# Optimization experiments

Measured on AMD Instinct MI355X. Metric: run time of the kernel, lower is better.

## Reference

```python
import jax, jax.numpy as jnp
import numpy as np

FIELD_NUM = 24

def _pair_indices(f):
    ii, jj = np.triu_indices(f, k=1)
    return jnp.asarray(ii), jnp.asarray(jj)

def setup_inputs() -> dict:
    key = jax.random.key(0)
    k1, k2 = jax.random.split(key)
    B, F, D = 16384, FIELD_NUM, 64
    P = F * (F - 1) // 2  # 276
    x = jax.random.normal(k1, (B, F, D), dtype=jnp.float32)
    W = jax.random.normal(k2, (P, D, D), dtype=jnp.float32) * 0.05
    return {"x": x, "W": W}

def reference(x, W):
    # x: (B, F, D) field embeddings; W: (P, D, D) per-pair bilinear matrices
    idx_i, idx_j = _pair_indices(FIELD_NUM)
    xi = x[:, idx_i, :]  # (B, P, D)
    xj = x[:, idx_j, :]  # (B, P, D)
    # sum_{p,d,e} xi[b,p,d] * W[p,d,e] * xj[b,p,e]
    logit = jnp.einsum('bpd,pde,bpe->b', xi, W, xj)
    return logit[:, None]  # (B, 1), matching tf output shape
```

## Files before the change

### kernel.cpp

```cpp
#include <hip/hip_runtime.h>
#include <stdint.h>

#define B_TOT 16384
#define F_NUM 24
#define P_NUM 276
#define BT    32
#define NTH   512
#define ROWP  1544

typedef float f32x16 __attribute__((ext_vector_type(16)));
typedef float f32x4  __attribute__((ext_vector_type(4)));
typedef short bf16x8 __attribute__((ext_vector_type(8)));

__device__ inline unsigned short f2bf(float f) {
    unsigned u = __float_as_uint(f);
    u += 0x7fffu + ((u >> 16) & 1u);
    return (unsigned short)(u >> 16);
}
__device__ inline float bf2f(unsigned short h) {
    return __uint_as_float(((unsigned)h) << 16);
}

struct Tab { int ent[8][36]; int cnt[8]; };
constexpr Tab build_tab() {
    Tab t{};
    int ii[276] = {}, jj[276] = {};
    int n = 0;
    for (int i = 0; i < 24; ++i)
        for (int j = i + 1; j < 24; ++j) { ii[n] = i; jj[n] = j; ++n; }
    int pos = 0;
    for (int w = 0; w < 8; ++w) {
        int c = (w < 2) ? 36 : 34;
        t.cnt[w] = c;
        for (int k = 0; k < c; ++k, ++pos) {
            int flag = (k == c - 1) || (ii[pos + 1] != ii[pos]);
            t.ent[w][k] = pos | (jj[pos] << 9) | (ii[pos] << 14) | (flag << 19);
        }
    }
    return t;
}
__device__ __constant__ Tab gtab = build_tab();

__global__ __launch_bounds__(256) void wprep(const float* __restrict__ W,
                                             unsigned short* __restrict__ afrag) {
    __shared__ __align__(16) unsigned short wlds[64 * 72];
    int p = blockIdx.x, t = threadIdx.x;
    const float4* src = (const float4*)(W + (size_t)p * 4096);
    #pragma unroll
    for (int c = 0; c < 4; ++c) {
        int i = t + c * 256;
        float4 v = src[i];
        int d = i >> 4;
        int e = (i & 15) * 4;
        ushort4 h; h.x=f2bf(v.x); h.y=f2bf(v.y); h.z=f2bf(v.z); h.w=f2bf(v.w);
        *(ushort4*)(&wlds[d * 72 + e]) = h;
    }
    __syncthreads();
    #pragma unroll
    for (int c = 0; c < 2; ++c) {
        int sl = t + c * 256;
        int u = sl >> 6, lane = sl & 63;
        int ks = u >> 1, m = u & 1;
        int d = m * 32 + (lane & 31);
        int e = ks * 16 + (lane >> 5) * 8;
        bf16x8 v = *(const bf16x8*)(&wlds[d * 72 + e]);
        *(bf16x8*)(afrag + ((size_t)(p * 8 + u) * 64 + lane) * 8) = v;
    }
}

#define MF(A_, B_, C_) __builtin_amdgcn_mfma_f32_32x32x16_bf16(A_, B_, C_, 0, 0, 0)

__device__ __forceinline__ void epilog(int e, const unsigned short* xrow, int q4,
                                       f32x16& a0, f32x16& a1, float& tacc) {
    int fi = (e >> 14) & 31;
    const unsigned short* ep = xrow + fi * 64 + q4;
    #pragma unroll
    for (int g = 0; g < 4; ++g) {
        ushort4 u0 = *(const ushort4*)(ep + 8 * g);
        tacc += a0[4*g+0]*bf2f(u0.x) + a0[4*g+1]*bf2f(u0.y)
              + a0[4*g+2]*bf2f(u0.z) + a0[4*g+3]*bf2f(u0.w);
        u0 = *(const ushort4*)(ep + 32 + 8 * g);
        tacc += a1[4*g+0]*bf2f(u0.x) + a1[4*g+1]*bf2f(u0.y)
              + a1[4*g+2]*bf2f(u0.z) + a1[4*g+3]*bf2f(u0.w);
    }
    #pragma unroll
    for (int k = 0; k < 16; ++k) { a0[k] = 0.f; a1[k] = 0.f; }
}

#define PSTEP(E_, NE_, C0,C1,C2,C3,C4,C5,C6,C7, X0,X1,X2,X3,                   \
                        N0,N1,N2,N3,N4,N5,N6,N7, Y0,Y1,Y2,Y3) do {             \
    { const bf16x8* ap_ = afr + (size_t)((NE_) & 511) * 512 + lane;            \
      N0 = ap_[0];   N1 = ap_[64];  N2 = ap_[128]; N3 = ap_[192];              \
      N4 = ap_[256]; N5 = ap_[320]; N6 = ap_[384]; N7 = ap_[448]; }            \
    { const unsigned short* bp_ = xrow + (((NE_) >> 9) & 31) * 64 + q8;        \
      Y0 = *(const bf16x8*)(bp_);      Y1 = *(const bf16x8*)(bp_ + 16);        \
      Y2 = *(const bf16x8*)(bp_ + 32); Y3 = *(const bf16x8*)(bp_ + 48); }      \
    __builtin_amdgcn_s_setprio(1);                                             \
    a0 = MF(C0, X0, a0); a1 = MF(C1, X0, a1);                                  \
    a0 = MF(C2, X1, a0); a1 = MF(C3, X1, a1);                                  \
    a0 = MF(C4, X2, a0); a1 = MF(C5, X2, a1);                                  \
    a0 = MF(C6, X3, a0); a1 = MF(C7, X3, a1);                                  \
    __builtin_amdgcn_s_setprio(0);                                             \
    if ((E_) & (1 << 19)) epilog(E_, xrow, q4, a0, a1, tacc);                  \
} while (0)

__global__ __launch_bounds__(NTH, 2) void fmfm_main(const float* __restrict__ x,
                                                    const unsigned short* __restrict__ afrag,
                                                    float* __restrict__ out) {
    __shared__ __align__(16) unsigned short xs[BT * ROWP];
    __shared__ float t_red[BT];
    const int tid = threadIdx.x;
    const int btile = blockIdx.x;
    const int lane = tid & 63;
    const int wv = __builtin_amdgcn_readfirstlane(tid >> 6);
    const int bcol = lane & 31;
    const int q = lane >> 5;
    const int q8 = q * 8, q4 = q * 4;

    if (tid < BT) t_red[tid] = 0.0f;

    const bf16x8* afr = (const bf16x8*)afrag;
    const unsigned short* xrow = xs + bcol * ROWP;

    float tacc = 0.f;
    f32x16 a0, a1;
    #pragma unroll
    for (int k = 0; k < 16; ++k) { a0[k] = 0.f; a1[k] = 0.f; }

    bf16x8 WA0,WA1,WA2,WA3,WA4,WA5,WA6,WA7;
    bf16x8 WB0,WB1,WB2,WB3,WB4,WB5,WB6,WB7;
    bf16x8 XA0,XA1,XA2,XA3;
    bf16x8 XB0,XB1,XB2,XB3;

    const int cnt = gtab.cnt[wv];
    const int ef  = gtab.ent[wv][0];
    { const bf16x8* ap = afr + (size_t)(ef & 511) * 512 + lane;
      WA0=ap[0];   WA1=ap[64];  WA2=ap[128]; WA3=ap[192];
      WA4=ap[256]; WA5=ap[320]; WA6=ap[384]; WA7=ap[448]; }

    const float* xg = x + (size_t)btile * BT * 1536;
    #pragma unroll 4
    for (int c = 0; c < 24; ++c) {
        int idx = tid + c * NTH;
        int row = idx / 384;
        int c4  = idx - row * 384;
        f32x4 v = __builtin_nontemporal_load(
                      (const f32x4*)(xg + (size_t)row * 1536 + c4 * 4));
        ushort4 h; h.x=f2bf(v.x); h.y=f2bf(v.y); h.z=f2bf(v.z); h.w=f2bf(v.w);
        *(ushort4*)(&xs[row * ROWP + c4 * 4]) = h;
    }
    __syncthreads();

    { const unsigned short* bp = xrow + ((ef >> 9) & 31) * 64 + q8;
      XA0 = *(const bf16x8*)(bp);      XA1 = *(const bf16x8*)(bp + 16);
      XA2 = *(const bf16x8*)(bp + 32); XA3 = *(const bf16x8*)(bp + 48); }

    #pragma unroll 1
    for (int s = 0; s < cnt; s += 2) {
        int e0 = gtab.ent[wv][s];
        int e1 = gtab.ent[wv][s + 1];
        int sn = (s + 2 < cnt) ? s + 2 : s + 1;
        int e2 = gtab.ent[wv][sn];
        PSTEP(e0, e1, WA0,WA1,WA2,WA3,WA4,WA5,WA6,WA7, XA0,XA1,XA2,XA3,
                      WB0,WB1,WB2,WB3,WB4,WB5,WB6,WB7, XB0,XB1,XB2,XB3);
        PSTEP(e1, e2, WB0,WB1,WB2,WB3,WB4,WB5,WB6,WB7, XB0,XB1,XB2,XB3,
                      WA0,WA1,WA2,WA3,WA4,WA5,WA6,WA7, XA0,XA1,XA2,XA3);
    }

    atomicAdd(&t_red[bcol], tacc);
    __syncthreads();
    if (tid < BT) out[(size_t)btile * BT + tid] = t_red[tid];
}

extern "C" void kernel_launch(void* const* d_in, const int* in_sizes, int n_in,
                              void* d_out, int out_size, void* d_ws, size_t ws_size,
                              hipStream_t stream) {
    const float* x = (const float*)d_in[0];
    const float* W = (const float*)d_in[1];
    float* out = (float*)d_out;
    unsigned short* afrag = (unsigned short*)d_ws;
    wprep<<<P_NUM, 256, 0, stream>>>(W, afrag);
    fmfm_main<<<B_TOT / BT, NTH, 0, stream>>>(x, afrag, out);
}
```

Measured before the change: 184.7 us.

## Split MFMA accumulators and hand-issue W loads with explicit vmcnt waits

Replaces the compiler-generated global loads of the W fragments with inline-asm dwordx4 loads and an explicit s_waitcnt vmcnt(8), so the next pair's W prefetch stays in flight while the current MFMAs run. The two accumulators per pair become four, breaking each dependent chain of four MFMAs into two chains of two, and the epilog sums the accumulator pairs. This aims to hide global-load latency and MFMA back-to-back dependency stalls. In exchange it uses more accumulator registers, which may pressure occupancy at two blocks per CU, and relies on manual wait counts that bypass the compiler's load tracking.

```diff
diff --git a/kernel.cpp b/kernel.cpp
--- a/kernel.cpp
+++ b/kernel.cpp
@@ -6,6 +6,7 @@
 #define P_NUM 276
 #define BT    32
 #define NTH   512
+#define NWV   8
 #define ROWP  1544
 
 typedef float f32x16 __attribute__((ext_vector_type(16)));
@@ -21,7 +22,7 @@
     return __uint_as_float(((unsigned)h) << 16);
 }
 
-struct Tab { int ent[8][36]; int cnt[8]; };
+struct Tab { int ent[NWV][36]; int cnt[NWV]; };
 constexpr Tab build_tab() {
     Tab t{};
     int ii[276] = {}, jj[276] = {};
@@ -29,7 +30,7 @@
     for (int i = 0; i < 24; ++i)
         for (int j = i + 1; j < 24; ++j) { ii[n] = i; jj[n] = j; ++n; }
     int pos = 0;
-    for (int w = 0; w < 8; ++w) {
+    for (int w = 0; w < NWV; ++w) {
         int c = (w < 2) ? 36 : 34;
         t.cnt[w] = c;
         for (int k = 0; k < c; ++k, ++pos) {
@@ -70,38 +71,64 @@
 
 #define MF(A_, B_, C_) __builtin_amdgcn_mfma_f32_32x32x16_bf16(A_, B_, C_, 0, 0, 0)
 
-__device__ __forceinline__ void epilog(int e, const unsigned short* xrow, int q4,
-                                       f32x16& a0, f32x16& a1, float& tacc) {
-    int fi = (e >> 14) & 31;
-    const unsigned short* ep = xrow + fi * 64 + q4;
-    #pragma unroll
-    for (int g = 0; g < 4; ++g) {
-        ushort4 u0 = *(const ushort4*)(ep + 8 * g);
-        tacc += a0[4*g+0]*bf2f(u0.x) + a0[4*g+1]*bf2f(u0.y)
-              + a0[4*g+2]*bf2f(u0.z) + a0[4*g+3]*bf2f(u0.w);
-        u0 = *(const ushort4*)(ep + 32 + 8 * g);
-        tacc += a1[4*g+0]*bf2f(u0.x) + a1[4*g+1]*bf2f(u0.y)
-              + a1[4*g+2]*bf2f(u0.z) + a1[4*g+3]*bf2f(u0.w);
-    }
-    #pragma unroll
-    for (int k = 0; k < 16; ++k) { a0[k] = 0.f; a1[k] = 0.f; }
-}
+#define GLDW8(P_, N0,N1,N2,N3,N4,N5,N6,N7) do {                                \
+    const bf16x8* b0_ = (P_);                                                  \
+    const bf16x8* b1_ = (P_) + 256;                                            \
+    asm volatile(                                                              \
+        "global_load_dwordx4 %0, %8, off\n\t"                                  \
+        "global_load_dwordx4 %1, %8, off offset:1024\n\t"                      \
+        "global_load_dwordx4 %2, %8, off offset:2048\n\t"                      \
+        "global_load_dwordx4 %3, %8, off offset:3072\n\t"                      \
+        "global_load_dwordx4 %4, %9, off\n\t"                                  \
+        "global_load_dwordx4 %5, %9, off offset:1024\n\t"                      \
+        "global_load_dwordx4 %6, %9, off offset:2048\n\t"                      \
+        "global_load_dwordx4 %7, %9, off offset:3072"                          \
+        : "=&v"(N0),"=&v"(N1),"=&v"(N2),"=&v"(N3),                             \
+          "=&v"(N4),"=&v"(N5),"=&v"(N6),"=&v"(N7)                              \
+        : "v"(b0_), "v"(b1_));                                                 \
+} while (0)
+
+#define EPI(E_) do {                                                           \
+    int fi_ = ((E_) >> 14) & 31;                                               \
+    const unsigned short* ep_ = xrow + fi_ * 64 + q4;                          \
+    _Pragma("unroll")                                                          \
+    for (int g_ = 0; g_ < 4; ++g_) {                                           \
+        ushort4 u_ = *(const ushort4*)(ep_ + 8 * g_);                          \
+        tacc += (a0[4*g_+0]+a2[4*g_+0])*bf2f(u_.x)                             \
+              + (a0[4*g_+1]+a2[4*g_+1])*bf2f(u_.y)                             \
+              + (a0[4*g_+2]+a2[4*g_+2])*bf2f(u_.z)                             \
+              + (a0[4*g_+3]+a2[4*g_+3])*bf2f(u_.w);                            \
+        u_ = *(const ushort4*)(ep_ + 32 + 8 * g_);                             \
+        tacc += (a1[4*g_+0]+a3[4*g_+0])*bf2f(u_.x)                             \
+              + (a1[4*g_+1]+a3[4*g_+1])*bf2f(u_.y)                             \
+              + (a1[4*g_+2]+a3[4*g_+2])*bf2f(u_.z)                             \
+              + (a1[4*g_+3]+a3[4*g_+3])*bf2f(u_.w);                            \
+    }                                                                          \
+    _Pragma("unroll")                                                          \
+    for (int k_ = 0; k_ < 16; ++k_) { a0[k_]=0.f; a1[k_]=0.f;                  \
+                                      a2[k_]=0.f; a3[k_]=0.f; }                \
+} while (0)
 
 #define PSTEP(E_, NE_, C0,C1,C2,C3,C4,C5,C6,C7, X0,X1,X2,X3,                   \
                         N0,N1,N2,N3,N4,N5,N6,N7, Y0,Y1,Y2,Y3) do {             \
-    { const bf16x8* ap_ = afr + (size_t)((NE_) & 511) * 512 + lane;            \
-      N0 = ap_[0];   N1 = ap_[64];  N2 = ap_[128]; N3 = ap_[192];              \
-      N4 = ap_[256]; N5 = ap_[320]; N6 = ap_[384]; N7 = ap_[448]; }            \
+    GLDW8(afr + (size_t)((NE_) & 511) * 512 + lane,                            \
+          N0,N1,N2,N3,N4,N5,N6,N7);                                            \
     { const unsigned short* bp_ = xrow + (((NE_) >> 9) & 31) * 64 + q8;        \
       Y0 = *(const bf16x8*)(bp_);      Y1 = *(const bf16x8*)(bp_ + 16);        \
       Y2 = *(const bf16x8*)(bp_ + 32); Y3 = *(const bf16x8*)(bp_ + 48); }      \
+    asm volatile("s_waitcnt vmcnt(8)");                                        \
+    __builtin_amdgcn_sched_barrier(0);                                         \
     __builtin_amdgcn_s_setprio(1);                                             \
-    a0 = MF(C0, X0, a0); a1 = MF(C1, X0, a1);                                  \
-    a0 = MF(C2, X1, a0); a1 = MF(C3, X1, a1);                                  \
-    a0 = MF(C4, X2, a0); a1 = MF(C5, X2, a1);                                  \
-    a0 = MF(C6, X3, a0); a1 = MF(C7, X3, a1);                                  \
+    a0 = MF(C0, X0, a0);                                          \
+    a1 = MF(C1, X0, a1);                                          \
+    a2 = MF(C4, X2, a2);                                          \
+    a3 = MF(C5, X2, a3);                                          \
+    a0 = MF(C2, X1, a0);                                          \
+    a1 = MF(C3, X1, a1);                                          \
+    a2 = MF(C6, X3, a2);                                          \
+    a3 = MF(C7, X3, a3);                                          \
     __builtin_amdgcn_s_setprio(0);                                             \
-    if ((E_) & (1 << 19)) epilog(E_, xrow, q4, a0, a1, tacc);                  \
+    if ((E_) & (1 << 19)) EPI(E_);                                             \
 } while (0)
 
 __global__ __launch_bounds__(NTH, 2) void fmfm_main(const float* __restrict__ x,
@@ -123,9 +150,9 @@
     const unsigned short* xrow = xs + bcol * ROWP;
 
     float tacc = 0.f;
-    f32x16 a0, a1;
+    f32x16 a0, a1, a2, a3;
     #pragma unroll
-    for (int k = 0; k < 16; ++k) { a0[k] = 0.f; a1[k] = 0.f; }
+    for (int k = 0; k < 16; ++k) { a0[k]=0.f; a1[k]=0.f; a2[k]=0.f; a3[k]=0.f; }
 
     bf16x8 WA0,WA1,WA2,WA3,WA4,WA5,WA6,WA7;
     bf16x8 WB0,WB1,WB2,WB3,WB4,WB5,WB6,WB7;
@@ -134,9 +161,8 @@
 
     const int cnt = gtab.cnt[wv];
     const int ef  = gtab.ent[wv][0];
-    { const bf16x8* ap = afr + (size_t)(ef & 511) * 512 + lane;
-      WA0=ap[0];   WA1=ap[64];  WA2=ap[128]; WA3=ap[192];
-      WA4=ap[256]; WA5=ap[320]; WA6=ap[384]; WA7=ap[448]; }
+    GLDW8(afr + (size_t)(ef & 511) * 512 + lane,
+          WA0,WA1,WA2,WA3,WA4,WA5,WA6,WA7);
 
     const float* xg = x + (size_t)btile * BT * 1536;
     #pragma unroll 4
@@ -146,7 +172,7 @@
         int c4  = idx - row * 384;
         f32x4 v = __builtin_nontemporal_load(
                       (const f32x4*)(xg + (size_t)row * 1536 + c4 * 4));
-        ushort4 h; h.x=f2bf(v.x); h.y=f2bf(v.y); h.z=f2bf(v.z); h.w=f2bf(v.w);
+        ushort4 h; h.x=f2bf(v[0]); h.y=f2bf(v[1]); h.z=f2bf(v[2]); h.w=f2bf(v[3]);
         *(ushort4*)(&xs[row * ROWP + c4 * 4]) = h;
     }
     __syncthreads();
@@ -166,6 +192,7 @@
         PSTEP(e1, e2, WB0,WB1,WB2,WB3,WB4,WB5,WB6,WB7, XB0,XB1,XB2,XB3,
                       WA0,WA1,WA2,WA3,WA4,WA5,WA6,WA7, XA0,XA1,XA2,XA3);
     }
+    asm volatile("s_waitcnt vmcnt(0)");
 
     atomicAdd(&t_red[bcol], tacc);
     __syncthreads();
```

New measurement: 183.8 us. About the same (-0.5%).
